# Optimization experiments

Measured on AMD Instinct MI355X. Metric: run time of the kernel, lower is better.

## Reference

```python
import jax, jax.numpy as jnp
import numpy as np

D_MODEL = 1024
N_HEADS = 16
HEAD_DIM = D_MODEL // N_HEADS


def setup_inputs() -> dict:
    key = jax.random.key(0)
    ks = jax.random.split(key, 10)
    B, S = 4, 2048
    scale = 1.0 / np.sqrt(D_MODEL)
    inp = {
        "x": jax.random.normal(ks[0], (B, S, D_MODEL), dtype=jnp.float32),
        "attention_mask": jnp.ones((B, S), dtype=jnp.int32),
        "Wq": jax.random.normal(ks[1], (D_MODEL, D_MODEL), dtype=jnp.float32) * scale,
        "bq": jnp.zeros((D_MODEL,), dtype=jnp.float32),
        "Wk": jax.random.normal(ks[2], (D_MODEL, D_MODEL), dtype=jnp.float32) * scale,
        "bk": jnp.zeros((D_MODEL,), dtype=jnp.float32),
        "Wv": jax.random.normal(ks[3], (D_MODEL, D_MODEL), dtype=jnp.float32) * scale,
        "bv": jnp.zeros((D_MODEL,), dtype=jnp.float32),
        "Wo": jax.random.normal(ks[4], (D_MODEL, D_MODEL), dtype=jnp.float32) * scale,
        "bo": jnp.zeros((D_MODEL,), dtype=jnp.float32),
    }
    return inp


def reference(x, attention_mask, Wq, bq, Wk, bk, Wv, bv, Wo, bo):
    B, S, _ = x.shape
    # projections, then split heads: [B, H, S, Dh]
    def proj(W, b):
        return (x @ W.T + b).reshape(B, S, N_HEADS, HEAD_DIM).transpose(0, 2, 1, 3)
    Q = proj(Wq, bq)
    K = proj(Wk, bk)
    V = proj(Wv, bv)
    # scores: [B, H, S, S]
    scores = jnp.einsum("bhqd,bhkd->bhqk", Q, K) / np.sqrt(HEAD_DIM)
    mask = attention_mask[:, None, None, :]  # [B,1,1,S]
    scores = jnp.where(mask == 0, -jnp.inf, scores)
    attn = jax.nn.softmax(scores, axis=-1)
    out = jnp.einsum("bhqk,bhkd->bhqd", attn, V)
    out = out.transpose(0, 2, 1, 3).reshape(B, S, D_MODEL)
    out = out @ Wo.T + bo
    return out
```

## Files before the change

### kernel.cpp

```cpp
#include <hip/hip_runtime.h>
#include <stdint.h>
#include <stddef.h>

typedef __attribute__((ext_vector_type(8))) short bf16x8;
typedef __attribute__((ext_vector_type(4))) float f32x4;

#define LOG2E 1.44269504088896340736f

__device__ __forceinline__ unsigned short f2bf(float f) {
  union { float f; unsigned u; } v; v.f = f;
  unsigned u = v.u + 0x7fffu + ((v.u >> 16) & 1u);
  return (unsigned short)(u >> 16);
}

__device__ __forceinline__ void gload_lds16(const void* g, void* l) {
  __builtin_amdgcn_global_load_lds(
      (const __attribute__((address_space(1))) unsigned int*)g,
      (__attribute__((address_space(3))) unsigned int*)l, 16, 0, 0);
}

__device__ __forceinline__ unsigned cvt_pk_bf16(float lo, float hi) {
  unsigned r;
  asm("v_cvt_pk_bf16_f32 %0, %1, %2" : "=v"(r) : "v"(lo), "v"(hi));
  return r;
}
__device__ __forceinline__ void pl32_swap(unsigned& a, unsigned& b) {
  asm("v_permlane32_swap_b32 %0, %1" : "+v"(a), "+v"(b));
}
__device__ __forceinline__ void pl16_swap(unsigned& a, unsigned& b) {
  asm("v_permlane16_swap_b32 %0, %1" : "+v"(a), "+v"(b));
}

__global__ void convert_all(const float* __restrict__ x,
                            const float* __restrict__ wq, const float* __restrict__ wk,
                            const float* __restrict__ wv, const float* __restrict__ wo,
                            const int* __restrict__ mask,
                            unsigned short* __restrict__ dst,
                            float* __restrict__ addm) {
  size_t i = ((size_t)blockIdx.x * 256 + threadIdx.x) * 4;
  if (i >= 12582912) {
    size_t j = i - 12582912;
    const int4 m = *(const int4*)(mask + j);
    float4 o;
    o.x = m.x ? 0.f : -1e30f;
    o.y = m.y ? 0.f : -1e30f;
    o.z = m.z ? 0.f : -1e30f;
    o.w = m.w ? 0.f : -1e30f;
    *(float4*)(addm + j) = o;
    return;
  }
  const float* src; size_t off;
  if (i < 8388608) { src = x; off = i; }
  else {
    size_t j = i - 8388608;
    int w = (int)(j >> 20);
    off = j & 1048575;
    src = (w == 0) ? wq : (w == 1) ? wk : (w == 2) ? wv : wo;
  }
  const float4 v = *(const float4*)(src + off);
  ushort4 o;
  o.x = f2bf(v.x); o.y = f2bf(v.y); o.z = f2bf(v.z); o.w = f2bf(v.w);
  *(ushort4*)(dst + i) = o;
}

template<int MODE>
__global__ __launch_bounds__(256, 2)
void gemm_bt(const unsigned short* __restrict__ A,
             const unsigned short* __restrict__ Bw,
             const float* __restrict__ bias,
             unsigned short* __restrict__ outb,
             float* __restrict__ outf,
             float scale) {
  __shared__ char lds[32768];
  const int t = threadIdx.x;
  const int lane = t & 63;
  const int wave = t >> 6;
  const int wr = wave >> 1, wc = wave & 1;
  const int bm = blockIdx.y << 7;
  const int bn = blockIdx.x << 7;

  f32x4 acc[4][4];
  for (int i = 0; i < 4; ++i)
    for (int j = 0; j < 4; ++j)
      for (int r = 0; r < 4; ++r) acc[i][j][r] = 0.f;

  for (int kt = 0; kt < 16; ++kt) {
    __syncthreads();
    {
      const size_t abase = ((size_t)bm * 1024 + (size_t)kt * 64) * 2;
      const size_t bbase = ((size_t)bn * 1024 + (size_t)kt * 64) * 2;
      for (int c = 0; c < 4; ++c) {
        const int o = (c << 12) + (t << 4);
        const int r = o >> 7;
        const int kb = o & 127;
        const int kbg = kb ^ ((r & 7) << 4);
        gload_lds16((const char*)A + abase + (size_t)r * 2048 + kbg, lds + o);
      }
      for (int c = 0; c < 4; ++c) {
        const int o = (c << 12) + (t << 4);
        const int r = o >> 7;
        const int kb = o & 127;
        const int kbg = kb ^ ((r & 7) << 4);
        gload_lds16((const char*)Bw + bbase + (size_t)r * 2048 + kbg, lds + 16384 + o);
      }
    }
    __syncthreads();
    for (int ks = 0; ks < 2; ++ks) {
      const int kbl = (ks << 6) + ((lane >> 4) << 4);
      bf16x8 af[4], bfr[4];
      for (int mf = 0; mf < 4; ++mf) {
        const int r = (wr << 6) + (mf << 4) + (lane & 15);
        af[mf] = *(const bf16x8*)(lds + (r << 7) + (kbl ^ ((r & 7) << 4)));
      }
      for (int nf = 0; nf < 4; ++nf) {
        const int r = (wc << 6) + (nf << 4) + (lane & 15);
        bfr[nf] = *(const bf16x8*)(lds + 16384 + (r << 7) + (kbl ^ ((r & 7) << 4)));
      }
      __builtin_amdgcn_s_setprio(1);
      for (int mf = 0; mf < 4; ++mf)
        for (int nf = 0; nf < 4; ++nf)
          acc[mf][nf] = __builtin_amdgcn_mfma_f32_16x16x32_bf16(af[mf], bfr[nf], acc[mf][nf], 0, 0, 0);
      __builtin_amdgcn_s_setprio(0);
    }
  }

  const int rsub = (lane >> 4) << 2;
  const int csub = lane & 15;
  for (int mf = 0; mf < 4; ++mf)
    for (int nf = 0; nf < 4; ++nf) {
      const int row0 = bm + (wr << 6) + (mf << 4) + rsub;
      const int col  = bn + (wc << 6) + (nf << 4) + csub;
      for (int rg = 0; rg < 4; ++rg) {
        const int row = row0 + rg;
        float v = acc[mf][nf][rg];
        if (MODE == 0) {
          v = (v + bias[col]) * scale;
          const int b = row >> 11, s = row & 2047, h = col >> 6, d = col & 63;
          size_t idx = ((size_t)((b << 4) + h) << 11) + (size_t)s;
          idx = (idx << 6) + (size_t)d;
          outb[idx] = f2bf(v);
        } else if (MODE == 2) {
          v = v + bias[row];
          const int b = col >> 11, s = col & 2047;
          const size_t idx = ((size_t)(b * 1024 + row) << 11) + (size_t)s;
          outb[idx] = f2bf(v);
        } else {
          v = v + bias[col];
          outf[(size_t)row * 1024 + (size_t)col] = v;
        }
      }
    }
}

__global__ __launch_bounds__(256, 2)
void attn_fwd(const unsigned short* __restrict__ Q,
              const unsigned short* __restrict__ K,
              const unsigned short* __restrict__ Vt,
              const float* __restrict__ addm,
              unsigned short* __restrict__ Aout) {
  __shared__ char lds[32768];
  const int t = threadIdx.x, lane = t & 63, wave = t >> 6;
  const int g = lane >> 4, m15 = lane & 15;
  const int blk = blockIdx.x;
  const int head = blk & 63, qt = blk >> 6;
  const int b = head >> 4, h = head & 15;
  const int qbase = qt << 7;
  const unsigned short* Qh = Q + ((size_t)head << 17);
  const unsigned short* Kh = K + ((size_t)head << 17);
  const unsigned short* Vh = Vt + ((size_t)head << 17);
  const float* amb = addm + (b << 11);

  bf16x8 aq[2][2];
  for (int rf = 0; rf < 2; ++rf)
    for (int ks = 0; ks < 2; ++ks) {
      const int row = qbase + (wave << 5) + (rf << 4) + m15;
      const int k = (ks << 5) + (g << 3);
      aq[rf][ks] = *(const bf16x8*)(Qh + ((size_t)row << 6) + (size_t)k);
    }

  f32x4 oacc[2][4];
  for (int i = 0; i < 2; ++i)
    for (int j = 0; j < 4; ++j)
      for (int r = 0; r < 4; ++r) oacc[i][j][r] = 0.f;
  float lsum[2] = {0.f, 0.f};

  for (int it = 0; it < 16; ++it) {
    const int kv = it << 7;
    __syncthreads();
    for (int c = 0; c < 4; ++c) {
      const int o = (c << 12) + (t << 4);
      const int r = o >> 7, kb = o & 127;
      gload_lds16((const char*)Kh + (((size_t)(kv + r)) << 7) + (size_t)(kb ^ ((r & 7) << 4)),
                  lds + o);
    }
    for (int c = 0; c < 4; ++c) {
      const int o = (c << 12) + (t << 4);
      const int d = o >> 8, kb = o & 255;
      gload_lds16((const char*)Vh + (((size_t)d) << 12) + (size_t)(kv << 1)
                      + (size_t)(kb ^ ((d & 7) << 4)),
                  lds + 16384 + o);
    }
    __syncthreads();

    float4 fm[8];
    for (int cf = 0; cf < 8; ++cf)
      fm[cf] = *(const float4*)(amb + kv + (cf << 4) + (g << 2));

    f32x4 s[2][8];
    for (int i = 0; i < 2; ++i)
      for (int j = 0; j < 8; ++j)
        for (int r = 0; r < 4; ++r) s[i][j][r] = 0.f;
    for (int ks = 0; ks < 2; ++ks) {
      const int kbl = (ks << 6) + (g << 4);
      bf16x8 bk[8];
      for (int cf = 0; cf < 8; ++cf) {
        const int r = (cf << 4) + m15;
        bk[cf] = *(const bf16x8*)(lds + (r << 7) + (kbl ^ ((r & 7) << 4)));
      }
      __builtin_amdgcn_s_setprio(1);
      for (int rf = 0; rf < 2; ++rf)
        for (int cf = 0; cf < 8; ++cf)
          s[rf][cf] = __builtin_amdgcn_mfma_f32_16x16x32_bf16(bk[cf], aq[rf][ks], s[rf][cf], 0, 0, 0);
      __builtin_amdgcn_s_setprio(0);
    }

    bf16x8 pa[2][4];
    for (int rf = 0; rf < 2; ++rf) {
      for (int cf = 0; cf < 8; ++cf)
        for (int rg = 0; rg < 4; ++rg) {
          const float p = __builtin_amdgcn_exp2f(s[rf][cf][rg] + fm[cf][rg]);
          lsum[rf] += p;
          s[rf][cf][rg] = p;
        }
      for (int k2 = 0; k2 < 4; ++k2) {
        const int ce = k2 << 1, co = ce + 1;
        unsigned A = cvt_pk_bf16(s[rf][ce][0], s[rf][ce][1]);
        unsigned B = cvt_pk_bf16(s[rf][ce][2], s[rf][ce][3]);
        unsigned C = cvt_pk_bf16(s[rf][co][0], s[rf][co][1]);
        unsigned D = cvt_pk_bf16(s[rf][co][2], s[rf][co][3]);
        pl32_swap(A, C);
        pl32_swap(B, D);
        pl16_swap(A, C);
        pl16_swap(B, D);
        union { unsigned u[4]; bf16x8 v; } pk;
        pk.u[0] = A; pk.u[1] = B; pk.u[2] = C; pk.u[3] = D;
        pa[rf][k2] = pk.v;
      }
    }

    for (int k2 = 0; k2 < 4; ++k2) {
      const int kbl = (k2 << 6) + (g << 4);
      bf16x8 bv[4];
      for (int cf = 0; cf < 4; ++cf) {
        const int d = (cf << 4) + m15;
        bv[cf] = *(const bf16x8*)(lds + 16384 + (d << 8) + (kbl ^ ((d & 7) << 4)));
      }
      __builtin_amdgcn_s_setprio(1);
      for (int rf = 0; rf < 2; ++rf)
        for (int cf = 0; cf < 4; ++cf)
          oacc[rf][cf] = __builtin_amdgcn_mfma_f32_16x16x32_bf16(pa[rf][k2], bv[cf], oacc[rf][cf], 0, 0, 0);
      __builtin_amdgcn_s_setprio(0);
    }
  }

  for (int rf = 0; rf < 2; ++rf) {
    float ls = lsum[rf];
    ls += __shfl_xor(ls, 16);
    ls += __shfl_xor(ls, 32);
    float inv[4];
    for (int rg = 0; rg < 4; ++rg)
      inv[rg] = 1.f / __shfl(ls, (g << 2) + rg);
    for (int cf = 0; cf < 4; ++cf)
      for (int rg = 0; rg < 4; ++rg)
        oacc[rf][cf][rg] *= inv[rg];
  }

  for (int rf = 0; rf < 2; ++rf)
    for (int cf = 0; cf < 4; ++cf)
      for (int rg = 0; rg < 4; ++rg) {
        const int q = qbase + (wave << 5) + (rf << 4) + (g << 2) + rg;
        const int d = (cf << 4) + m15;
        Aout[(((size_t)(b << 11) + q) << 10) + (size_t)((h << 6) + d)] = f2bf(oacc[rf][cf][rg]);
      }
}

extern "C" void kernel_launch(void* const* d_in, const int* in_sizes, int n_in,
                              void* d_out, int out_size, void* d_ws, size_t ws_size,
                              hipStream_t stream) {
  const float* x  = (const float*)d_in[0];
  const int* mask = (const int*)d_in[1];
  const float* Wq = (const float*)d_in[2];
  const float* bq = (const float*)d_in[3];
  const float* Wk = (const float*)d_in[4];
  const float* bk = (const float*)d_in[5];
  const float* Wv = (const float*)d_in[6];
  const float* bv = (const float*)d_in[7];
  const float* Wo = (const float*)d_in[8];
  const float* bo = (const float*)d_in[9];
  float* out = (float*)d_out;

  unsigned short* xb  = (unsigned short*)d_ws;
  unsigned short* wqb = xb  + 8388608;
  unsigned short* wkb = wqb + 1048576;
  unsigned short* wvb = wkb + 1048576;
  unsigned short* wob = wvb + 1048576;
  unsigned short* Qb  = wob + 1048576;
  unsigned short* Kb  = Qb  + 8388608;
  unsigned short* Vtb = Kb  + 8388608;
  unsigned short* Ab  = Vtb + 8388608;
  float* addm = (float*)(Ab + 8388608);

  convert_all<<<12296, 256, 0, stream>>>(x, Wq, Wk, Wv, Wo, mask, xb, addm);
  const float qscale = 0.125f * LOG2E;
  gemm_bt<0><<<dim3(8, 64), 256, 0, stream>>>(xb, wqb, bq, Qb, nullptr, qscale);
  gemm_bt<0><<<dim3(8, 64), 256, 0, stream>>>(xb, wkb, bk, Kb, nullptr, 1.0f);
  gemm_bt<2><<<dim3(64, 8), 256, 0, stream>>>(wvb, xb, bv, Vtb, nullptr, 1.0f);
  attn_fwd<<<1024, 256, 0, stream>>>(Qb, Kb, Vtb, addm, Ab);
  gemm_bt<3><<<dim3(8, 64), 256, 0, stream>>>(Ab, wob, bo, nullptr, out, 1.0f);
}
```

Baseline: 283.0 us.

## Fuse Q, K, V projections into one GEMM launch over concatenated weights

Result: no change. 277.5 us (-2.0%).

```diff
diff --git a/kernel.cpp b/kernel.cpp
--- a/kernel.cpp
+++ b/kernel.cpp
@@ -63,14 +63,14 @@
   *(ushort4*)(dst + i) = o;
 }
 
-template<int MODE>
 __global__ __launch_bounds__(256, 2)
-void gemm_bt(const unsigned short* __restrict__ A,
-             const unsigned short* __restrict__ Bw,
-             const float* __restrict__ bias,
-             unsigned short* __restrict__ outb,
-             float* __restrict__ outf,
-             float scale) {
+void gemm_qkv(const unsigned short* __restrict__ A,
+              const unsigned short* __restrict__ Bw,
+              const float* __restrict__ bq, const float* __restrict__ bk,
+              const float* __restrict__ bv,
+              unsigned short* __restrict__ Qb, unsigned short* __restrict__ Kb,
+              unsigned short* __restrict__ Vtb,
+              float qscale) {
   __shared__ char lds[32768];
   const int t = threadIdx.x;
   const int lane = t & 63;
@@ -124,31 +124,115 @@
     }
   }
 
+  const int seg = bn >> 10;
+  const float* bias = (seg == 0) ? bq : (seg == 1) ? bk : bv;
+  const float scale = (seg == 0) ? qscale : 1.0f;
+  const int rsub = (lane >> 4) << 2;
+  const int csub = lane & 15;
+
+  if (seg < 2) {
+    unsigned short* outp = (seg == 0) ? Qb : Kb;
+    for (int mf = 0; mf < 4; ++mf)
+      for (int nf = 0; nf < 4; ++nf) {
+        const int row0 = bm + (wr << 6) + (mf << 4) + rsub;
+        const int c1 = ((bn + (wc << 6) + (nf << 4) + csub) & 1023);
+        const float bb = bias[c1];
+        const int h = c1 >> 6, d = c1 & 63;
+        for (int rg = 0; rg < 4; ++rg) {
+          const int row = row0 + rg;
+          const float v = (acc[mf][nf][rg] + bb) * scale;
+          const int b = row >> 11, s = row & 2047;
+          size_t idx = ((size_t)((b << 4) + h) << 11) + (size_t)s;
+          idx = (idx << 6) + (size_t)d;
+          outp[idx] = f2bf(v);
+        }
+      }
+  } else {
+    for (int mf = 0; mf < 4; ++mf)
+      for (int nf = 0; nf < 4; ++nf) {
+        const int row0 = bm + (wr << 6) + (mf << 4) + rsub;
+        const int c1 = ((bn + (wc << 6) + (nf << 4) + csub) & 1023);
+        const float bb = bias[c1];
+        const int h = c1 >> 6, d = c1 & 63;
+        const int b = row0 >> 11, s = row0 & 2047;
+        ushort4 w;
+        w.x = f2bf(acc[mf][nf][0] + bb);
+        w.y = f2bf(acc[mf][nf][1] + bb);
+        w.z = f2bf(acc[mf][nf][2] + bb);
+        w.w = f2bf(acc[mf][nf][3] + bb);
+        const size_t idx = (((size_t)((b << 4) + h) << 6) + (size_t)d) << 11;
+        *(ushort4*)(Vtb + idx + (size_t)s) = w;
+      }
+  }
+}
+
+__global__ __launch_bounds__(256, 2)
+void gemm_out(const unsigned short* __restrict__ A,
+              const unsigned short* __restrict__ Bw,
+              const float* __restrict__ bias,
+              float* __restrict__ outf) {
+  __shared__ char lds[32768];
+  const int t = threadIdx.x;
+  const int lane = t & 63;
+  const int wave = t >> 6;
+  const int wr = wave >> 1, wc = wave & 1;
+  const int bm = blockIdx.y << 7;
+  const int bn = blockIdx.x << 7;
+
+  f32x4 acc[4][4];
+  for (int i = 0; i < 4; ++i)
+    for (int j = 0; j < 4; ++j)
+      for (int r = 0; r < 4; ++r) acc[i][j][r] = 0.f;
+
+  for (int kt = 0; kt < 16; ++kt) {
+    __syncthreads();
+    {
+      const size_t abase = ((size_t)bm * 1024 + (size_t)kt * 64) * 2;
+      const size_t bbase = ((size_t)bn * 1024 + (size_t)kt * 64) * 2;
+      for (int c = 0; c < 4; ++c) {
+        const int o = (c << 12) + (t << 4);
+        const int r = o >> 7;
+        const int kb = o & 127;
+        const int kbg = kb ^ ((r & 7) << 4);
+        gload_lds16((const char*)A + abase + (size_t)r * 2048 + kbg, lds + o);
+      }
+      for (int c = 0; c < 4; ++c) {
+        const int o = (c << 12) + (t << 4);
+        const int r = o >> 7;
+        const int kb = o & 127;
+        const int kbg = kb ^ ((r & 7) << 4);
+        gload_lds16((const char*)Bw + bbase + (size_t)r * 2048 + kbg, lds + 16384 + o);
+      }
+    }
+    __syncthreads();
+    for (int ks = 0; ks < 2; ++ks) {
+      const int kbl = (ks << 6) + ((lane >> 4) << 4);
+      bf16x8 af[4], bfr[4];
+      for (int mf = 0; mf < 4; ++mf) {
+        const int r = (wr << 6) + (mf << 4) + (lane & 15);
+        af[mf] = *(const bf16x8*)(lds + (r << 7) + (kbl ^ ((r & 7) << 4)));
+      }
+      for (int nf = 0; nf < 4; ++nf) {
+        const int r = (wc << 6) + (nf << 4) + (lane & 15);
+        bfr[nf] = *(const bf16x8*)(lds + 16384 + (r << 7) + (kbl ^ ((r & 7) << 4)));
+      }
+      __builtin_amdgcn_s_setprio(1);
+      for (int mf = 0; mf < 4; ++mf)
+        for (int nf = 0; nf < 4; ++nf)
+          acc[mf][nf] = __builtin_amdgcn_mfma_f32_16x16x32_bf16(af[mf], bfr[nf], acc[mf][nf], 0, 0, 0);
+      __builtin_amdgcn_s_setprio(0);
+    }
+  }
+
   const int rsub = (lane >> 4) << 2;
   const int csub = lane & 15;
   for (int mf = 0; mf < 4; ++mf)
     for (int nf = 0; nf < 4; ++nf) {
       const int row0 = bm + (wr << 6) + (mf << 4) + rsub;
       const int col  = bn + (wc << 6) + (nf << 4) + csub;
-      for (int rg = 0; rg < 4; ++rg) {
-        const int row = row0 + rg;
-        float v = acc[mf][nf][rg];
-        if (MODE == 0) {
-          v = (v + bias[col]) * scale;
-          const int b = row >> 11, s = row & 2047, h = col >> 6, d = col & 63;
-          size_t idx = ((size_t)((b << 4) + h) << 11) + (size_t)s;
-          idx = (idx << 6) + (size_t)d;
-          outb[idx] = f2bf(v);
-        } else if (MODE == 2) {
-          v = v + bias[row];
-          const int b = col >> 11, s = col & 2047;
-          const size_t idx = ((size_t)(b * 1024 + row) << 11) + (size_t)s;
-          outb[idx] = f2bf(v);
-        } else {
-          v = v + bias[col];
-          outf[(size_t)row * 1024 + (size_t)col] = v;
-        }
-      }
+      const float bb = bias[col];
+      for (int rg = 0; rg < 4; ++rg)
+        outf[(size_t)(row0 + rg) * 1024 + (size_t)col] = acc[mf][nf][rg] + bb;
     }
 }
 
@@ -301,9 +385,7 @@
 
   unsigned short* xb  = (unsigned short*)d_ws;
   unsigned short* wqb = xb  + 8388608;
-  unsigned short* wkb = wqb + 1048576;
-  unsigned short* wvb = wkb + 1048576;
-  unsigned short* wob = wvb + 1048576;
+  unsigned short* wob = wqb + 3145728;
   unsigned short* Qb  = wob + 1048576;
   unsigned short* Kb  = Qb  + 8388608;
   unsigned short* Vtb = Kb  + 8388608;
@@ -312,9 +394,7 @@
 
   convert_all<<<12296, 256, 0, stream>>>(x, Wq, Wk, Wv, Wo, mask, xb, addm);
   const float qscale = 0.125f * LOG2E;
-  gemm_bt<0><<<dim3(8, 64), 256, 0, stream>>>(xb, wqb, bq, Qb, nullptr, qscale);
-  gemm_bt<0><<<dim3(8, 64), 256, 0, stream>>>(xb, wkb, bk, Kb, nullptr, 1.0f);
-  gemm_bt<2><<<dim3(64, 8), 256, 0, stream>>>(wvb, xb, bv, Vtb, nullptr, 1.0f);
+  gemm_qkv<<<dim3(24, 64), 256, 0, stream>>>(xb, wqb, bq, bk, bv, Qb, Kb, Vtb, qscale);
   attn_fwd<<<1024, 256, 0, stream>>>(Qb, Kb, Vtb, addm, Ab);
-  gemm_bt<3><<<dim3(8, 64), 256, 0, stream>>>(Ab, wob, bo, nullptr, out, 1.0f);
-}
+  gemm_out<<<dim3(8, 64), 256, 0, stream>>>(Ab, wob, bo, out);
+}
```
